# Performance work log

Hardware: AMD Instinct MI355X
Metric: run time of the kernel (lower is better)

## Reference

```python
import jax, jax.numpy as jnp
import numpy as np

N = 50000   # nodes
E = 800000  # edges (before self loops)
IN_DIM = 64
HID = 128
HEADS = 4
DH = HID // HEADS  # 32 per-head out_feats
L = 3
EPS = 1e-5
NEG_SLOPE = 0.2


def setup_inputs() -> dict:
    key = jax.random.key(0)
    ks = jax.random.split(key, 10)
    s = 0.1  # weight scale for numerical sanity
    return {
        "node_feats": jax.random.normal(ks[0], (N, IN_DIM), jnp.float32),
        "src": jax.random.randint(ks[1], (E,), 0, N, dtype=jnp.int32),
        "dst": jax.random.randint(ks[2], (E,), 0, N, dtype=jnp.int32),
        "W_in": jax.random.normal(ks[3], (IN_DIM, HID), jnp.float32) * s,
        "b_in": jnp.zeros((HID,), jnp.float32),
        "W_src": jax.random.normal(ks[4], (L, HID, HID), jnp.float32) * s,
        "b_src": jnp.zeros((L, HID), jnp.float32),
        "W_dst": jax.random.normal(ks[5], (L, HID, HID), jnp.float32) * s,
        "b_dst": jnp.zeros((L, HID), jnp.float32),
        "attn": jax.random.normal(ks[6], (L, HEADS, DH), jnp.float32) * s,
        "ln_g": jnp.ones((L, HID), jnp.float32),
        "ln_b": jnp.zeros((L, HID), jnp.float32),
    }


def _layer_norm(x, g, b):
    mu = jnp.mean(x, axis=-1, keepdims=True)
    var = jnp.mean((x - mu) ** 2, axis=-1, keepdims=True)
    return (x - mu) * jax.lax.rsqrt(var + EPS) * g + b


def _gatv2(h, s_idx, d_idx, Ws, bs, Wd, bd, a):
    # h: [N, HID]; edges s_idx -> d_idx (self loops included)
    fs = (h @ Ws + bs).reshape(N, HEADS, DH)  # W_src h, source features
    fd = (h @ Wd + bd).reshape(N, HEADS, DH)  # W_dst h, dest features
    e = jax.nn.leaky_relu(fs[s_idx] + fd[d_idx], NEG_SLOPE)   # [E', H, D]
    logits = jnp.einsum('ehd,hd->eh', e, a)                   # [E', H]
    # segment softmax over incoming edges of each destination node
    m = jax.ops.segment_max(logits, d_idx, num_segments=N)    # [N, H]
    p = jnp.exp(logits - m[d_idx])
    z = jax.ops.segment_sum(p, d_idx, num_segments=N)         # [N, H]
    alpha = p / z[d_idx]                                      # [E', H]
    msg = fs[s_idx] * alpha[..., None]                        # [E', H, D]
    out = jax.ops.segment_sum(msg, d_idx, num_segments=N)     # [N, H, D]
    out = out + h.reshape(N, HEADS, DH)  # residual (Identity res_fc)
    return out.reshape(N, HID)


def reference(node_feats, src, dst, W_in, b_in, W_src, b_src, W_dst, b_dst, attn, ln_g, ln_b):
    loop = jnp.arange(N, dtype=src.dtype)
    s_idx = jnp.concatenate([src, loop])  # add_self_loop
    d_idx = jnp.concatenate([dst, loop])
    h = node_feats @ W_in + b_in
    for l in range(L):
        h_new = _gatv2(h, s_idx, d_idx, W_src[l], b_src[l], W_dst[l], b_dst[l], attn[l])
        h = _layer_norm(h + h_new, ln_g[l], ln_b[l])
        h = jax.nn.relu(h)
    graph_emb = jnp.mean(h, axis=0, keepdims=True)  # dgl.mean_nodes, batch of 1 graph
    return graph_emb, h
```

## Files before the change

kernel.cpp:

```cpp
#include <hip/hip_runtime.h>
#include <hip/hip_bf16.h>

#define NN 50000
#define NPAIR 25000
#define CSH 13
#define CHUNK (1 << CSH)

typedef short short8 __attribute__((ext_vector_type(8)));
typedef float f32x4 __attribute__((ext_vector_type(4)));

#define GLOBAL_AS __attribute__((address_space(1)))
#define LDS_AS __attribute__((address_space(3)))

__device__ __forceinline__ unsigned short f2bf(float f) {
    unsigned int b = __float_as_uint(f);
    unsigned int r = (b + 0x7FFFu + ((b >> 16) & 1u)) >> 16;
    return (unsigned short)r;
}
__device__ __forceinline__ float bf2f(unsigned short u) {
    return __uint_as_float((unsigned int)u << 16);
}
__device__ __forceinline__ float4 bfu4(ushort4 u) {
    float4 v;
    v.x = bf2f(u.x); v.y = bf2f(u.y); v.z = bf2f(u.z); v.w = bf2f(u.w);
    return v;
}
__device__ __forceinline__ float edge_logit(float4 v, float4 fd4, float4 a06, float4 a04) {
    float e0 = v.x + fd4.x, e1 = v.y + fd4.y, e2 = v.z + fd4.z, e3 = v.w + fd4.w;
    return e0 * a06.x + fabsf(e0) * a04.x + e1 * a06.y + fabsf(e1) * a04.y
         + e2 * a06.z + fabsf(e2) * a04.z + e3 * a06.w + fabsf(e3) * a04.w;
}

__global__ __launch_bounds__(256) void hist_kernel(const int* __restrict__ dst,
                                                   unsigned* __restrict__ cntmat,
                                                   int* __restrict__ rank, int E) {
    __shared__ unsigned pc[NPAIR];
    int b = blockIdx.x, tid = threadIdx.x;
    for (int k = tid; k < NPAIR; k += 256) pc[k] = 0;
    __syncthreads();
    int beg = b << CSH;
    int end = beg + CHUNK; if (end > E) end = E;
    for (int i = beg + tid; i < end; i += 256) {
        int d = dst[i];
        unsigned sh = (unsigned)(d & 1) << 4;
        unsigned old = atomicAdd(&pc[d >> 1], 1u << sh);
        rank[i] = (int)((old >> sh) & 0xffffu);
    }
    __syncthreads();
    unsigned* o = cntmat + (size_t)b * NPAIR;
    for (int k = tid; k < NPAIR; k += 256) o[k] = pc[k];
}

__global__ __launch_bounds__(256, 4) void prep2_kernel(
        unsigned* __restrict__ cntmat, int HB,
        int* __restrict__ counts, int* __restrict__ row_beg, int* total,
        const float* __restrict__ Ws, const float* __restrict__ Wd,
        unsigned short* __restrict__ WtL,
        const float* __restrict__ x, const float* __restrict__ Win,
        const float* __restrict__ bin, unsigned short* __restrict__ hB) {
    const int PB = (NPAIR + 255) / 256;
    int blk = blockIdx.x, tid = threadIdx.x;
    if (blk < PB) {
        int p = blk * 256 + tid;
        unsigned run = 0;
        if (p < NPAIR) {
            size_t idx = p;
            #pragma unroll 4
            for (int b = 0; b < HB; ++b, idx += NPAIR) {
                unsigned c = cntmat[idx];
                cntmat[idx] = run;
                run += c;
            }
        }
        int c0 = (int)(run & 0xffffu), c1 = (int)(run >> 16);
        int lane = tid & 63;
        int len = (p < NPAIR) ? (c0 + c1 + 2) : 0;
        int pscan = len;
        #pragma unroll
        for (int off = 1; off < 64; off <<= 1) {
            int t = __shfl_up(pscan, off);
            if (lane >= off) pscan += t;
        }
        int tot = __shfl(pscan, 63);
        int base = 0;
        if (lane == 63) base = atomicAdd(total, tot);
        base = __shfl(base, 63);
        if (p < NPAIR) {
            int rb = base + pscan - len;
            counts[2 * p] = c0;
            counts[2 * p + 1] = c1;
            row_beg[2 * p] = rb;
            row_beg[2 * p + 1] = rb + c0 + 1;
        }
        return;
    }
    int w = tid >> 6, l = tid & 63;
    int m = l & 15, q = l >> 4;
    if (blk < PB + 384) {
        int e = (blk - PB) * 256 + tid;
        int ll = e >> 15;
        int r = e & 32767;
        int colc = r >> 7;
        int k = r & 127;
        float v = (colc < 128) ? Ws[ll * 16384 + k * 128 + colc]
                               : Wd[ll * 16384 + k * 128 + (colc - 128)];
        WtL[ll * 32768 + colc * 128 + k] = f2bf(v);
        return;
    }
    int blk0 = blk - PB - 384;
    short8 B[2][2];
    #pragma unroll
    for (int ct = 0; ct < 2; ++ct) {
        int colw = w * 32 + ct * 16 + m;
        #pragma unroll
        for (int kt = 0; kt < 2; ++kt) {
            short8 a;
            #pragma unroll
            for (int jj = 0; jj < 8; ++jj)
                a[jj] = (short)f2bf(Win[(kt * 32 + q * 8 + jj) * 128 + colw]);
            B[ct][kt] = a;
        }
    }
    float bias[2];
    #pragma unroll
    for (int ct = 0; ct < 2; ++ct) bias[ct] = bin[w * 32 + ct * 16 + m];
    for (int rg = blk0; rg < NN / 16; rg += 512) {
        int row0 = rg * 16;
        const float* ap = x + (size_t)(row0 + m) * 64 + q * 8;
        short8 A[2];
        #pragma unroll
        for (int kt = 0; kt < 2; ++kt) {
            float4 f0 = *(const float4*)(ap + kt * 32);
            float4 f1 = *(const float4*)(ap + kt * 32 + 4);
            short8 a;
            a[0] = (short)f2bf(f0.x); a[1] = (short)f2bf(f0.y);
            a[2] = (short)f2bf(f0.z); a[3] = (short)f2bf(f0.w);
            a[4] = (short)f2bf(f1.x); a[5] = (short)f2bf(f1.y);
            a[6] = (short)f2bf(f1.z); a[7] = (short)f2bf(f1.w);
            A[kt] = a;
        }
        f32x4 acc[2];
        #pragma unroll
        for (int ct = 0; ct < 2; ++ct) acc[ct] = (f32x4){0.f, 0.f, 0.f, 0.f};
        #pragma unroll
        for (int kt = 0; kt < 2; ++kt)
            #pragma unroll
            for (int ct = 0; ct < 2; ++ct)
                acc[ct] = __builtin_amdgcn_mfma_f32_16x16x32_bf16(A[kt], B[ct][kt], acc[ct], 0, 0, 0);
        #pragma unroll
        for (int ct = 0; ct < 2; ++ct) {
            int colw = w * 32 + ct * 16 + m;
            #pragma unroll
            for (int i = 0; i < 4; ++i) {
                int row = row0 + q * 4 + i;
                hB[(size_t)row * 128 + colw] = f2bf(acc[ct][i] + bias[ct]);
            }
        }
    }
}

__device__ __forceinline__ void dual_body(const unsigned short* __restrict__ hB,
                                          const unsigned short* __restrict__ Wt,
                                          const float* __restrict__ bs,
                                          const float* __restrict__ bd,
                                          unsigned short* __restrict__ fsB,
                                          unsigned short* __restrict__ fdB,
                                          unsigned short* Atile, int t0, int tstride) {
    int tid = threadIdx.x;
    int w = tid >> 6, l = tid & 63;
    int m = l & 15, q = l >> 4;
    short8 B[4][4];
    #pragma unroll
    for (int ct = 0; ct < 4; ++ct) {
        int colw = w * 64 + ct * 16 + m;
        const unsigned short* wp = Wt + colw * 128 + q * 8;
        #pragma unroll
        for (int kt = 0; kt < 4; ++kt) B[ct][kt] = *(const short8*)(wp + kt * 32);
    }
    const float* bptr = (w < 2) ? bs : bd;
    unsigned short* OUT = (w < 2) ? fsB : fdB;
    int ocb = (w * 64) & 127;
    float bias[4];
    #pragma unroll
    for (int ct = 0; ct < 4; ++ct) bias[ct] = bptr[ocb + ct * 16 + m];

    const int NT = (NN + 63) / 64;
    for (int t = t0; t < NT; t += tstride) {
        int row0 = t * 64;
        const char* gsrc = (const char*)(hB + (size_t)row0 * 128);
        #pragma unroll
        for (int c = 0; c < 4; ++c) {
            int off = c * 4096 + tid * 16;
            __builtin_amdgcn_global_load_lds((const GLOBAL_AS void*)(gsrc + off),
                                             (LDS_AS void*)((char*)Atile + off), 16, 0, 0);
        }
        __syncthreads();
        #pragma unroll
        for (int rg = 0; rg < 4; ++rg) {
            const unsigned short* ap = Atile + (rg * 16 + m) * 128 + q * 8;
            short8 A[4];
            #pragma unroll
            for (int kt = 0; kt < 4; ++kt) A[kt] = *(const short8*)(ap + kt * 32);
            f32x4 acc[4];
            #pragma unroll
            for (int ct = 0; ct < 4; ++ct) acc[ct] = (f32x4){0.f, 0.f, 0.f, 0.f};
            #pragma unroll
            for (int kt = 0; kt < 4; ++kt)
                #pragma unroll
                for (int ct = 0; ct < 4; ++ct)
                    acc[ct] = __builtin_amdgcn_mfma_f32_16x16x32_bf16(A[kt], B[ct][kt], acc[ct], 0, 0, 0);
            #pragma unroll
            for (int ct = 0; ct < 4; ++ct) {
                int colw = ocb + ct * 16 + m;
                #pragma unroll
                for (int i = 0; i < 4; ++i) {
                    int row = row0 + rg * 16 + q * 4 + i;
                    if (row < NN) OUT[(size_t)row * 128 + colw] = f2bf(acc[ct][i] + bias[ct]);
                }
            }
        }
        __syncthreads();
    }
}

__global__ __launch_bounds__(256, 4) void scatter_dual_kernel(
        const int* __restrict__ src, const int* __restrict__ dst,
        const int* __restrict__ rank, const int* __restrict__ row_beg,
        const int* __restrict__ counts, const unsigned* __restrict__ cntmat,
        int* __restrict__ col, int E, int n,
        const unsigned short* __restrict__ hB, const unsigned short* __restrict__ Wt,
        const float* __restrict__ bs, const float* __restrict__ bd,
        unsigned short* __restrict__ fsB, unsigned short* __restrict__ fdB) {
    __shared__ unsigned short Atile[64 * 128];
    int SB = (E + n + 255) >> 8;
    if ((int)blockIdx.x < SB) {
        int i = blockIdx.x * 256 + threadIdx.x;
        if (i >= E + n) return;
        if (i < E) {
            int d = dst[i];
            int b = i >> CSH;
            unsigned pk = cntmat[(size_t)b * NPAIR + (d >> 1)];
            int off = (int)((pk >> ((unsigned)(d & 1) << 4)) & 0xffffu);
            col[row_beg[d] + off + rank[i]] = src[i];
        } else {
            int v = i - E;
            col[row_beg[v] + counts[v]] = v;
        }
        return;
    }
    dual_body(hB, Wt, bs, bd, fsB, fdB, Atile, blockIdx.x - SB, gridDim.x - SB);
}

__global__ __launch_bounds__(256, 4) void dual_gemm_mfma(const unsigned short* __restrict__ hB,
                                                         const unsigned short* __restrict__ Wt,
                                                         const float* __restrict__ bs,
                                                         const float* __restrict__ bd,
                                                         unsigned short* __restrict__ fsB,
                                                         unsigned short* __restrict__ fdB) {
    __shared__ unsigned short Atile[64 * 128];
    dual_body(hB, Wt, bs, bd, fsB, fdB, Atile, blockIdx.x, gridDim.x);
}

__global__ __launch_bounds__(256) void agg_ln_kernel(const unsigned short* __restrict__ h_in,
                                                     const unsigned short* __restrict__ fsB,
                                                     const unsigned short* __restrict__ fdB,
                                                     const int* __restrict__ row_beg,
                                                     const int* __restrict__ counts,
                                                     const int* __restrict__ col,
                                                     const float* __restrict__ attn,
                                                     const float* __restrict__ ln_g,
                                                     const float* __restrict__ ln_b,
                                                     unsigned short* __restrict__ hb_out,
                                                     float* __restrict__ hf_out, int n) {
    int gwave = (blockIdx.x * blockDim.x + threadIdx.x) >> 6;
    int lane = threadIdx.x & 63;
    int half = lane >> 5;
    int sub = lane & 31;
    int node = gwave * 2 + half;
    if (node >= n) return;
    int f0 = 4 * sub;
    unsigned foff = (unsigned)(f0 * 2);
    const char* fsp = (const char*)fsB;
    float4 fd4 = bfu4(*(const ushort4*)((const char*)fdB + (((unsigned)node << 8) | foff)));
    float4 h4 = bfu4(*(const ushort4*)((const char*)h_in + (((unsigned)node << 8) | foff)));
    const float4 a4 = *(const float4*)(attn + f0);
    float4 a06, a04;
    a06.x = 0.6f * a4.x; a06.y = 0.6f * a4.y; a06.z = 0.6f * a4.z; a06.w = 0.6f * a4.w;
    a04.x = 0.4f * a4.x; a04.y = 0.4f * a4.y; a04.z = 0.4f * a4.z; a04.w = 0.4f * a4.w;
    int beg = row_beg[node], end = beg + counts[node] + 1;

    float z[4];
    float4 acc[4];
    #pragma unroll
    for (int k = 0; k < 4; ++k) {
        z[k] = 0.f;
        acc[k].x = 0.f; acc[k].y = 0.f; acc[k].z = 0.f; acc[k].w = 0.f;
    }

    int j = beg;
    for (; j + 3 < end; j += 4) {
        int s0 = col[j], s1 = col[j + 1], s2 = col[j + 2], s3 = col[j + 3];
        ushort4 u0 = *(const ushort4*)(fsp + (((unsigned)s0 << 8) | foff));
        ushort4 u1 = *(const ushort4*)(fsp + (((unsigned)s1 << 8) | foff));
        ushort4 u2 = *(const ushort4*)(fsp + (((unsigned)s2 << 8) | foff));
        ushort4 u3 = *(const ushort4*)(fsp + (((unsigned)s3 << 8) | foff));
        float4 v0 = bfu4(u0), v1 = bfu4(u1), v2 = bfu4(u2), v3 = bfu4(u3);
        float p0 = edge_logit(v0, fd4, a06, a04);
        float p1 = edge_logit(v1, fd4, a06, a04);
        float p2 = edge_logit(v2, fd4, a06, a04);
        float p3 = edge_logit(v3, fd4, a06, a04);
        #pragma unroll
        for (int off = 1; off <= 4; off <<= 1) {
            p0 += __shfl_xor(p0, off); p1 += __shfl_xor(p1, off);
            p2 += __shfl_xor(p2, off); p3 += __shfl_xor(p3, off);
        }
        float w0 = __expf(p0), w1 = __expf(p1), w2 = __expf(p2), w3 = __expf(p3);
        z[0] += w0; z[1] += w1; z[2] += w2; z[3] += w3;
        acc[0].x += w0 * v0.x; acc[0].y += w0 * v0.y; acc[0].z += w0 * v0.z; acc[0].w += w0 * v0.w;
        acc[1].x += w1 * v1.x; acc[1].y += w1 * v1.y; acc[1].z += w1 * v1.z; acc[1].w += w1 * v1.w;
        acc[2].x += w2 * v2.x; acc[2].y += w2 * v2.y; acc[2].z += w2 * v2.z; acc[2].w += w2 * v2.w;
        acc[3].x += w3 * v3.x; acc[3].y += w3 * v3.y; acc[3].z += w3 * v3.z; acc[3].w += w3 * v3.w;
    }
    for (; j < end; ++j) {
        int s = col[j];
        ushort4 u = *(const ushort4*)(fsp + (((unsigned)s << 8) | foff));
        float4 v = bfu4(u);
        float p = edge_logit(v, fd4, a06, a04);
        p += __shfl_xor(p, 1);
        p += __shfl_xor(p, 2);
        p += __shfl_xor(p, 4);
        float w = __expf(p);
        z[0] += w;
        acc[0].x += w * v.x; acc[0].y += w * v.y; acc[0].z += w * v.z; acc[0].w += w * v.w;
    }
    float zT = (z[0] + z[1]) + (z[2] + z[3]);
    float axT = (acc[0].x + acc[1].x) + (acc[2].x + acc[3].x);
    float ayT = (acc[0].y + acc[1].y) + (acc[2].y + acc[3].y);
    float azT = (acc[0].z + acc[1].z) + (acc[2].z + acc[3].z);
    float awT = (acc[0].w + acc[1].w) + (acc[2].w + acc[3].w);
    float inv = 1.0f / zT;
    float x0 = 2.f * h4.x + axT * inv;
    float x1 = 2.f * h4.y + ayT * inv;
    float x2 = 2.f * h4.z + azT * inv;
    float x3 = 2.f * h4.w + awT * inv;
    float s = (x0 + x1) + (x2 + x3);
    #pragma unroll
    for (int off = 1; off <= 16; off <<= 1) s += __shfl_xor(s, off);
    float mean = s * (1.f / 128.f);
    float d0 = x0 - mean, d1 = x1 - mean, d2 = x2 - mean, d3 = x3 - mean;
    float v = (d0 * d0 + d1 * d1) + (d2 * d2 + d3 * d3);
    #pragma unroll
    for (int off = 1; off <= 16; off <<= 1) v += __shfl_xor(v, off);
    float rstd = rsqrtf(v * (1.f / 128.f) + 1e-5f);
    float4 g4 = *(const float4*)(ln_g + f0);
    float4 bb4 = *(const float4*)(ln_b + f0);
    float4 o;
    o.x = fmaxf(d0 * rstd * g4.x + bb4.x, 0.f);
    o.y = fmaxf(d1 * rstd * g4.y + bb4.y, 0.f);
    o.z = fmaxf(d2 * rstd * g4.z + bb4.z, 0.f);
    o.w = fmaxf(d3 * rstd * g4.w + bb4.w, 0.f);
    if (hf_out) {
        *(float4*)((char*)hf_out + (((unsigned)node << 9) | (unsigned)(f0 * 4))) = o;
    } else {
        ushort4 ob;
        ob.x = f2bf(o.x); ob.y = f2bf(o.y); ob.z = f2bf(o.z); ob.w = f2bf(o.w);
        *(ushort4*)((char*)hb_out + (((unsigned)node << 8) | foff)) = ob;
    }
}


__global__ __launch_bounds__(128) void mean1_kernel(const float* __restrict__ h,
                                                    float* __restrict__ partials, int n) {
    int c = threadIdx.x;
    float acc = 0.f;
    for (int r = blockIdx.x; r < n; r += gridDim.x)
        acc += h[(size_t)r * 128 + c];
    partials[blockIdx.x * 128 + c] = acc;
}

__global__ __launch_bounds__(1024) void mean2_kernel(const float* __restrict__ partials,
                                                     float* __restrict__ out, int nb, int n) {
    __shared__ float smem[8][128];
    int c = threadIdx.x & 127;
    int g = threadIdx.x >> 7;
    float acc = 0.f;
    for (int r = g; r < nb; r += 8)
        acc += partials[r * 128 + c];
    smem[g][c] = acc;
    __syncthreads();
    if (threadIdx.x < 128) {
        float s = 0.f;
        #pragma unroll
        for (int k = 0; k < 8; ++k) s += smem[k][c];
        out[c] = s * (1.f / n);
    }
}

extern "C" void kernel_launch(void* const* d_in, const int* in_sizes, int n_in,
                              void* d_out, int out_size, void* d_ws, size_t ws_size,
                              hipStream_t stream) {
    const float* node_feats = (const float*)d_in[0];
    const int* src = (const int*)d_in[1];
    const int* dst = (const int*)d_in[2];
    const float* W_in = (const float*)d_in[3];
    const float* b_in = (const float*)d_in[4];
    const float* W_src = (const float*)d_in[5];
    const float* b_src = (const float*)d_in[6];
    const float* W_dst = (const float*)d_in[7];
    const float* b_dst = (const float*)d_in[8];
    const float* attn = (const float*)d_in[9];
    const float* ln_g = (const float*)d_in[10];
    const float* ln_b = (const float*)d_in[11];
    float* out = (float*)d_out;

    const int N = NN;
    const int E = in_sizes[1];
    const int HB = (E + CHUNK - 1) >> CSH;

    unsigned short* fsB = (unsigned short*)d_ws;
    unsigned short* fdB = fsB + (size_t)N * 128;
    unsigned short* hB = fdB + (size_t)N * 128;
    unsigned short* WtL = hB + (size_t)N * 128;
    unsigned short* WtIn = WtL + 3 * 32768;
    int* counts = (int*)(WtIn + 8192);
    int* total = counts + N;
    int* row_beg = total + 1;
    int* rankb = row_beg + N;
    int* colb = rankb + E;
    unsigned* cntmat = (unsigned*)(colb + (E + N));
    float* partials = (float*)(cntmat + (size_t)HB * NPAIR);

    const int NT = (N + 63) / 64;

    hipMemsetAsync(total, 0, sizeof(int), stream);

    hist_kernel<<<HB, 256, 0, stream>>>(dst, cntmat, rankb, E);

    const int PB = (NPAIR + 255) / 256;
    prep2_kernel<<<PB + 384 + 512, 256, 0, stream>>>(cntmat, HB, counts, row_beg, total,
                                                     W_src, W_dst, WtL,
                                                     node_feats, W_in, b_in, hB);

    int SB = (E + N + 255) / 256;
    scatter_dual_kernel<<<SB + NT, 256, 0, stream>>>(src, dst, rankb, row_beg,
                                                     counts, cntmat, colb, E, N,
                                                     hB, WtL, b_src, b_dst, fsB, fdB);

    for (int l = 0; l < 3; ++l) {
        int last = (l == 2);
        if (l > 0)
            dual_gemm_mfma<<<NT, 256, 0, stream>>>(hB, WtL + (size_t)l * 32768,
                                                   b_src + l * 128, b_dst + l * 128,
                                                   fsB, fdB);
        agg_ln_kernel<<<(N + 7) / 8, 256, 0, stream>>>(hB, fsB, fdB, row_beg, counts, colb,
                                                       attn + l * 128, ln_g + l * 128,
                                                       ln_b + l * 128,
                                                       last ? nullptr : hB,
                                                       last ? (out + 128) : nullptr, N);
    }

    mean1_kernel<<<256, 128, 0, stream>>>(out + 128, partials, N);
    mean2_kernel<<<1, 1024, 0, stream>>>(partials, out, 256, N);
}
```

Baseline: 390.9 us.

## Fuse next-layer dual projection GEMM into aggregation/LayerNorm epilogue

The aggregation + LayerNorm kernel now processes 16 nodes per 512-thread block. It stages the bf16 output rows in shared memory, then runs an MFMA epilogue that computes the next layer's source and destination projections (plus bias) for those rows. Ping-pong fs/fd buffers in extra workspace let a layer read its inputs while writing the next layer's. This drops the separate dual_gemm launches and the re-read of h between layers. In exchange, every block re-loads the full 128x256 weight slice from cache and adds a block-wide barrier after an irregular gather. The fused path only runs when the workspace is large enough.

```diff
diff --git a/kernel.cpp b/kernel.cpp
--- a/kernel.cpp
+++ b/kernel.cpp
@@ -261,7 +261,7 @@
     dual_body(hB, Wt, bs, bd, fsB, fdB, Atile, blockIdx.x, gridDim.x);
 }
 
-__global__ __launch_bounds__(256) void agg_ln_kernel(const unsigned short* __restrict__ h_in,
+__global__ __launch_bounds__(512) void agg_ln_kernel(const unsigned short* __restrict__ h_in,
                                                      const unsigned short* __restrict__ fsB,
                                                      const unsigned short* __restrict__ fdB,
                                                      const int* __restrict__ row_beg,
@@ -271,100 +271,140 @@
                                                      const float* __restrict__ ln_g,
                                                      const float* __restrict__ ln_b,
                                                      unsigned short* __restrict__ hb_out,
-                                                     float* __restrict__ hf_out, int n) {
-    int gwave = (blockIdx.x * blockDim.x + threadIdx.x) >> 6;
-    int lane = threadIdx.x & 63;
+                                                     float* __restrict__ hf_out,
+                                                     const unsigned short* __restrict__ Wt2,
+                                                     const float* __restrict__ bs2,
+                                                     const float* __restrict__ bd2,
+                                                     unsigned short* __restrict__ fs_out,
+                                                     unsigned short* __restrict__ fd_out,
+                                                     int n) {
+    __shared__ unsigned short Otile[16 * 128];
+    int tid = threadIdx.x;
+    int wid = tid >> 6;
+    int lane = tid & 63;
     int half = lane >> 5;
     int sub = lane & 31;
-    int node = gwave * 2 + half;
-    if (node >= n) return;
+    int node = blockIdx.x * 16 + wid * 2 + half;
     int f0 = 4 * sub;
-    unsigned foff = (unsigned)(f0 * 2);
-    const char* fsp = (const char*)fsB;
-    float4 fd4 = bfu4(*(const ushort4*)((const char*)fdB + (((unsigned)node << 8) | foff)));
-    float4 h4 = bfu4(*(const ushort4*)((const char*)h_in + (((unsigned)node << 8) | foff)));
-    const float4 a4 = *(const float4*)(attn + f0);
-    float4 a06, a04;
-    a06.x = 0.6f * a4.x; a06.y = 0.6f * a4.y; a06.z = 0.6f * a4.z; a06.w = 0.6f * a4.w;
-    a04.x = 0.4f * a4.x; a04.y = 0.4f * a4.y; a04.z = 0.4f * a4.z; a04.w = 0.4f * a4.w;
-    int beg = row_beg[node], end = beg + counts[node] + 1;
-
-    float z[4];
-    float4 acc[4];
-    #pragma unroll
-    for (int k = 0; k < 4; ++k) {
-        z[k] = 0.f;
-        acc[k].x = 0.f; acc[k].y = 0.f; acc[k].z = 0.f; acc[k].w = 0.f;
-    }
-
-    int j = beg;
-    for (; j + 3 < end; j += 4) {
-        int s0 = col[j], s1 = col[j + 1], s2 = col[j + 2], s3 = col[j + 3];
-        ushort4 u0 = *(const ushort4*)(fsp + (((unsigned)s0 << 8) | foff));
-        ushort4 u1 = *(const ushort4*)(fsp + (((unsigned)s1 << 8) | foff));
-        ushort4 u2 = *(const ushort4*)(fsp + (((unsigned)s2 << 8) | foff));
-        ushort4 u3 = *(const ushort4*)(fsp + (((unsigned)s3 << 8) | foff));
-        float4 v0 = bfu4(u0), v1 = bfu4(u1), v2 = bfu4(u2), v3 = bfu4(u3);
-        float p0 = edge_logit(v0, fd4, a06, a04);
-        float p1 = edge_logit(v1, fd4, a06, a04);
-        float p2 = edge_logit(v2, fd4, a06, a04);
-        float p3 = edge_logit(v3, fd4, a06, a04);
-        #pragma unroll
-        for (int off = 1; off <= 4; off <<= 1) {
-            p0 += __shfl_xor(p0, off); p1 += __shfl_xor(p1, off);
-            p2 += __shfl_xor(p2, off); p3 += __shfl_xor(p3, off);
-        }
-        float w0 = __expf(p0), w1 = __expf(p1), w2 = __expf(p2), w3 = __expf(p3);
-        z[0] += w0; z[1] += w1; z[2] += w2; z[3] += w3;
-        acc[0].x += w0 * v0.x; acc[0].y += w0 * v0.y; acc[0].z += w0 * v0.z; acc[0].w += w0 * v0.w;
-        acc[1].x += w1 * v1.x; acc[1].y += w1 * v1.y; acc[1].z += w1 * v1.z; acc[1].w += w1 * v1.w;
-        acc[2].x += w2 * v2.x; acc[2].y += w2 * v2.y; acc[2].z += w2 * v2.z; acc[2].w += w2 * v2.w;
-        acc[3].x += w3 * v3.x; acc[3].y += w3 * v3.y; acc[3].z += w3 * v3.z; acc[3].w += w3 * v3.w;
-    }
-    for (; j < end; ++j) {
-        int s = col[j];
-        ushort4 u = *(const ushort4*)(fsp + (((unsigned)s << 8) | foff));
-        float4 v = bfu4(u);
-        float p = edge_logit(v, fd4, a06, a04);
-        p += __shfl_xor(p, 1);
-        p += __shfl_xor(p, 2);
-        p += __shfl_xor(p, 4);
-        float w = __expf(p);
-        z[0] += w;
-        acc[0].x += w * v.x; acc[0].y += w * v.y; acc[0].z += w * v.z; acc[0].w += w * v.w;
-    }
-    float zT = (z[0] + z[1]) + (z[2] + z[3]);
-    float axT = (acc[0].x + acc[1].x) + (acc[2].x + acc[3].x);
-    float ayT = (acc[0].y + acc[1].y) + (acc[2].y + acc[3].y);
-    float azT = (acc[0].z + acc[1].z) + (acc[2].z + acc[3].z);
-    float awT = (acc[0].w + acc[1].w) + (acc[2].w + acc[3].w);
-    float inv = 1.0f / zT;
-    float x0 = 2.f * h4.x + axT * inv;
-    float x1 = 2.f * h4.y + ayT * inv;
-    float x2 = 2.f * h4.z + azT * inv;
-    float x3 = 2.f * h4.w + awT * inv;
-    float s = (x0 + x1) + (x2 + x3);
-    #pragma unroll
-    for (int off = 1; off <= 16; off <<= 1) s += __shfl_xor(s, off);
-    float mean = s * (1.f / 128.f);
-    float d0 = x0 - mean, d1 = x1 - mean, d2 = x2 - mean, d3 = x3 - mean;
-    float v = (d0 * d0 + d1 * d1) + (d2 * d2 + d3 * d3);
-    #pragma unroll
-    for (int off = 1; off <= 16; off <<= 1) v += __shfl_xor(v, off);
-    float rstd = rsqrtf(v * (1.f / 128.f) + 1e-5f);
-    float4 g4 = *(const float4*)(ln_g + f0);
-    float4 bb4 = *(const float4*)(ln_b + f0);
-    float4 o;
-    o.x = fmaxf(d0 * rstd * g4.x + bb4.x, 0.f);
-    o.y = fmaxf(d1 * rstd * g4.y + bb4.y, 0.f);
-    o.z = fmaxf(d2 * rstd * g4.z + bb4.z, 0.f);
-    o.w = fmaxf(d3 * rstd * g4.w + bb4.w, 0.f);
-    if (hf_out) {
-        *(float4*)((char*)hf_out + (((unsigned)node << 9) | (unsigned)(f0 * 4))) = o;
-    } else {
+    if (node < n) {
+        unsigned foff = (unsigned)(f0 * 2);
+        const char* fsp = (const char*)fsB;
+        float4 fd4 = bfu4(*(const ushort4*)((const char*)fdB + (((unsigned)node << 8) | foff)));
+        float4 h4 = bfu4(*(const ushort4*)((const char*)h_in + (((unsigned)node << 8) | foff)));
+        const float4 a4 = *(const float4*)(attn + f0);
+        float4 a06, a04;
+        a06.x = 0.6f * a4.x; a06.y = 0.6f * a4.y; a06.z = 0.6f * a4.z; a06.w = 0.6f * a4.w;
+        a04.x = 0.4f * a4.x; a04.y = 0.4f * a4.y; a04.z = 0.4f * a4.z; a04.w = 0.4f * a4.w;
+        int beg = row_beg[node], end = beg + counts[node] + 1;
+
+        float z[4];
+        float4 acc[4];
+        #pragma unroll
+        for (int k = 0; k < 4; ++k) {
+            z[k] = 0.f;
+            acc[k].x = 0.f; acc[k].y = 0.f; acc[k].z = 0.f; acc[k].w = 0.f;
+        }
+
+        int j = beg;
+        for (; j + 3 < end; j += 4) {
+            int s0 = col[j], s1 = col[j + 1], s2 = col[j + 2], s3 = col[j + 3];
+            ushort4 u0 = *(const ushort4*)(fsp + (((unsigned)s0 << 8) | foff));
+            ushort4 u1 = *(const ushort4*)(fsp + (((unsigned)s1 << 8) | foff));
+            ushort4 u2 = *(const ushort4*)(fsp + (((unsigned)s2 << 8) | foff));
+            ushort4 u3 = *(const ushort4*)(fsp + (((unsigned)s3 << 8) | foff));
+            float4 v0 = bfu4(u0), v1 = bfu4(u1), v2 = bfu4(u2), v3 = bfu4(u3);
+            float p0 = edge_logit(v0, fd4, a06, a04);
+            float p1 = edge_logit(v1, fd4, a06, a04);
+            float p2 = edge_logit(v2, fd4, a06, a04);
+            float p3 = edge_logit(v3, fd4, a06, a04);
+            #pragma unroll
+            for (int off = 1; off <= 4; off <<= 1) {
+                p0 += __shfl_xor(p0, off); p1 += __shfl_xor(p1, off);
+                p2 += __shfl_xor(p2, off); p3 += __shfl_xor(p3, off);
+            }
+            float w0 = __expf(p0), w1 = __expf(p1), w2 = __expf(p2), w3 = __expf(p3);
+            z[0] += w0; z[1] += w1; z[2] += w2; z[3] += w3;
+            acc[0].x += w0 * v0.x; acc[0].y += w0 * v0.y; acc[0].z += w0 * v0.z; acc[0].w += w0 * v0.w;
+            acc[1].x += w1 * v1.x; acc[1].y += w1 * v1.y; acc[1].z += w1 * v1.z; acc[1].w += w1 * v1.w;
+            acc[2].x += w2 * v2.x; acc[2].y += w2 * v2.y; acc[2].z += w2 * v2.z; acc[2].w += w2 * v2.w;
+            acc[3].x += w3 * v3.x; acc[3].y += w3 * v3.y; acc[3].z += w3 * v3.z; acc[3].w += w3 * v3.w;
+        }
+        for (; j < end; ++j) {
+            int s = col[j];
+            ushort4 u = *(const ushort4*)(fsp + (((unsigned)s << 8) | foff));
+            float4 v = bfu4(u);
+            float p = edge_logit(v, fd4, a06, a04);
+            p += __shfl_xor(p, 1);
+            p += __shfl_xor(p, 2);
+            p += __shfl_xor(p, 4);
+            float w = __expf(p);
+            z[0] += w;
+            acc[0].x += w * v.x; acc[0].y += w * v.y; acc[0].z += w * v.z; acc[0].w += w * v.w;
+        }
+        float zT = (z[0] + z[1]) + (z[2] + z[3]);
+        float axT = (acc[0].x + acc[1].x) + (acc[2].x + acc[3].x);
+        float ayT = (acc[0].y + acc[1].y) + (acc[2].y + acc[3].y);
+        float azT = (acc[0].z + acc[1].z) + (acc[2].z + acc[3].z);
+        float awT = (acc[0].w + acc[1].w) + (acc[2].w + acc[3].w);
+        float inv = 1.0f / zT;
+        float x0 = 2.f * h4.x + axT * inv;
+        float x1 = 2.f * h4.y + ayT * inv;
+        float x2 = 2.f * h4.z + azT * inv;
+        float x3 = 2.f * h4.w + awT * inv;
+        float s = (x0 + x1) + (x2 + x3);
+        #pragma unroll
+        for (int off = 1; off <= 16; off <<= 1) s += __shfl_xor(s, off);
+        float mean = s * (1.f / 128.f);
+        float d0 = x0 - mean, d1 = x1 - mean, d2 = x2 - mean, d3 = x3 - mean;
+        float v = (d0 * d0 + d1 * d1) + (d2 * d2 + d3 * d3);
+        #pragma unroll
+        for (int off = 1; off <= 16; off <<= 1) v += __shfl_xor(v, off);
+        float rstd = rsqrtf(v * (1.f / 128.f) + 1e-5f);
+        float4 g4 = *(const float4*)(ln_g + f0);
+        float4 bb4 = *(const float4*)(ln_b + f0);
+        float4 o;
+        o.x = fmaxf(d0 * rstd * g4.x + bb4.x, 0.f);
+        o.y = fmaxf(d1 * rstd * g4.y + bb4.y, 0.f);
+        o.z = fmaxf(d2 * rstd * g4.z + bb4.z, 0.f);
+        o.w = fmaxf(d3 * rstd * g4.w + bb4.w, 0.f);
         ushort4 ob;
         ob.x = f2bf(o.x); ob.y = f2bf(o.y); ob.z = f2bf(o.z); ob.w = f2bf(o.w);
-        *(ushort4*)((char*)hb_out + (((unsigned)node << 8) | foff)) = ob;
+        if (hf_out) {
+            *(float4*)((char*)hf_out + (((unsigned)node << 9) | (unsigned)(f0 * 4))) = o;
+        } else {
+            *(ushort4*)((char*)hb_out + (((unsigned)node << 8) | foff)) = ob;
+        }
+        if (Wt2) {
+            *(ushort4*)(Otile + (wid * 2 + half) * 128 + f0) = ob;
+        }
+    }
+    if (!Wt2) return;
+    __syncthreads();
+    int m = lane & 15, q = lane >> 4;
+    int wcol = wid * 32;
+    const float* bptr = (wid < 4) ? bs2 : bd2;
+    unsigned short* OUT = (wid < 4) ? fs_out : fd_out;
+    int cbase = wcol & 127;
+    short8 A[4];
+    #pragma unroll
+    for (int kt = 0; kt < 4; ++kt)
+        A[kt] = *(const short8*)(Otile + m * 128 + q * 8 + kt * 32);
+    #pragma unroll
+    for (int ct = 0; ct < 2; ++ct) {
+        int colw = wcol + ct * 16 + m;
+        const unsigned short* wp = Wt2 + colw * 128 + q * 8;
+        f32x4 acc2 = (f32x4){0.f, 0.f, 0.f, 0.f};
+        #pragma unroll
+        for (int kt = 0; kt < 4; ++kt) {
+            short8 B = *(const short8*)(wp + kt * 32);
+            acc2 = __builtin_amdgcn_mfma_f32_16x16x32_bf16(A[kt], B, acc2, 0, 0, 0);
+        }
+        float bias = bptr[cbase + ct * 16 + m];
+        #pragma unroll
+        for (int i = 0; i < 4; ++i) {
+            int row = blockIdx.x * 16 + q * 4 + i;
+            if (row < n) OUT[(size_t)row * 128 + cbase + ct * 16 + m] = f2bf(acc2[i] + bias);
+        }
     }
 }
 
@@ -417,9 +457,9 @@
     const int E = in_sizes[1];
     const int HB = (E + CHUNK - 1) >> CSH;
 
-    unsigned short* fsB = (unsigned short*)d_ws;
-    unsigned short* fdB = fsB + (size_t)N * 128;
-    unsigned short* hB = fdB + (size_t)N * 128;
+    unsigned short* fsA = (unsigned short*)d_ws;
+    unsigned short* fdA = fsA + (size_t)N * 128;
+    unsigned short* hB = fdA + (size_t)N * 128;
     unsigned short* WtL = hB + (size_t)N * 128;
     unsigned short* WtIn = WtL + 3 * 32768;
     int* counts = (int*)(WtIn + 8192);
@@ -429,6 +469,10 @@
     int* colb = rankb + E;
     unsigned* cntmat = (unsigned*)(colb + (E + N));
     float* partials = (float*)(cntmat + (size_t)HB * NPAIR);
+    unsigned short* fs2 = (unsigned short*)(partials + 256 * 128);
+    unsigned short* fd2 = fs2 + (size_t)N * 128;
+    size_t need = (size_t)((char*)(fd2 + (size_t)N * 128) - (char*)d_ws);
+    int fused = (ws_size >= need);
 
     const int NT = (N + 63) / 64;
 
@@ -444,19 +488,27 @@
     int SB = (E + N + 255) / 256;
     scatter_dual_kernel<<<SB + NT, 256, 0, stream>>>(src, dst, rankb, row_beg,
                                                      counts, cntmat, colb, E, N,
-                                                     hB, WtL, b_src, b_dst, fsB, fdB);
+                                                     hB, WtL, b_src, b_dst, fsA, fdA);
 
     for (int l = 0; l < 3; ++l) {
         int last = (l == 2);
-        if (l > 0)
+        const unsigned short* fs_in = (fused && l == 1) ? fs2 : fsA;
+        const unsigned short* fd_in = (fused && l == 1) ? fd2 : fdA;
+        unsigned short* fs_o = (l == 0) ? fs2 : fsA;
+        unsigned short* fd_o = (l == 0) ? fd2 : fdA;
+        if (!fused && l > 0)
             dual_gemm_mfma<<<NT, 256, 0, stream>>>(hB, WtL + (size_t)l * 32768,
                                                    b_src + l * 128, b_dst + l * 128,
-                                                   fsB, fdB);
-        agg_ln_kernel<<<(N + 7) / 8, 256, 0, stream>>>(hB, fsB, fdB, row_beg, counts, colb,
-                                                       attn + l * 128, ln_g + l * 128,
-                                                       ln_b + l * 128,
-                                                       last ? nullptr : hB,
-                                                       last ? (out + 128) : nullptr, N);
+                                                   fsA, fdA);
+        agg_ln_kernel<<<(N + 15) / 16, 512, 0, stream>>>(
+            hB, fs_in, fd_in, row_beg, counts, colb,
+            attn + l * 128, ln_g + l * 128, ln_b + l * 128,
+            last ? nullptr : hB,
+            last ? (out + 128) : nullptr,
+            (fused && !last) ? (WtL + (size_t)(l + 1) * 32768) : nullptr,
+            b_src + (l + 1 < 3 ? l + 1 : 0) * 128,
+            b_dst + (l + 1 < 3 ? l + 1 : 0) * 128,
+            fs_o, fd_o, N);
     }
 
     mean1_kernel<<<256, 128, 0, stream>>>(out + 128, partials, N);
```

Result: slower. 460.2 us (+17.7%).
